# Kernel optimization log

Hardware: AMD Instinct MI355X
Metric: run time of the kernel (lower is better)

Reference implementation:

```python
import jax, jax.numpy as jnp
import numpy as np

S, B, C = 7, 2, 20
L_COORD, POS_CONF, POS_CLS, L_NOOBJ = 5.0, 1.0, 1.0, 0.5
IMG_SIZE, GRID_SIZE = 448.0, 64.0
EPS = 1e-6


def setup_inputs() -> dict:
    key = jax.random.key(0)
    k1, k2 = jax.random.split(key)
    N = 16384
    predictions = jax.random.uniform(k1, (N, S, S, B * 5 + C), dtype=jnp.float32)
    target = jax.random.uniform(k2, (N, S, S, 5 + C), dtype=jnp.float32)
    return {"predictions": predictions, "target": target}


def _iou(pred_boxes, gt_boxes, gx, gy):
    # pred_boxes: [N,S,S,B,4] (x,y offsets in cell, w,h rel. to image)
    # gt_boxes:   [N,S,S,1,4]
    # gx, gy:     broadcastable grid indices [1,S,S,1]
    def corners(b):
        cx = (gx + b[..., 0]) * GRID_SIZE   # absolute center x (pixels)
        cy = (gy + b[..., 1]) * GRID_SIZE
        w = b[..., 2] * IMG_SIZE
        h = b[..., 3] * IMG_SIZE
        return cx - w / 2, cy - h / 2, cx + w / 2, cy + h / 2, w * h

    px1, py1, px2, py2, pa = corners(pred_boxes)
    gx1, gy1, gx2, gy2, ga = corners(gt_boxes)
    iw = jnp.clip(jnp.minimum(px2, gx2) - jnp.maximum(px1, gx1), 0.0)
    ih = jnp.clip(jnp.minimum(py2, gy2) - jnp.maximum(py1, gy1), 0.0)
    inter = iw * ih
    union = pa + ga - inter
    return inter / (union + EPS)   # [N,S,S,B]


def reference(predictions, target):
    N = predictions.shape[0]
    pred_boxes = predictions[..., : B * 5].reshape(N, S, S, B, 5)
    pred_cls = predictions[..., B * 5:]          # [N,S,S,C]
    gt_box = target[..., :5][..., None, :]       # [N,S,S,1,5]
    gt_cls = target[..., 5:]                     # [N,S,S,C]

    obj = (target[..., 4] > 0.5).astype(predictions.dtype)  # [N,S,S]

    gx = jnp.arange(S, dtype=predictions.dtype)[None, None, :, None]  # col index
    gy = jnp.arange(S, dtype=predictions.dtype)[None, :, None, None]  # row index

    iou = _iou(pred_boxes[..., :4], gt_box[..., :4], gx, gy)  # [N,S,S,B]

    # responsible box: max-IoU predictor per obj cell
    resp = jax.nn.one_hot(jnp.argmax(iou, axis=-1), B, dtype=predictions.dtype)  # [N,S,S,B]
    resp_obj = resp * obj[..., None]

    # coordinate loss (x, y, sqrt(w), sqrt(h))
    dxy = jnp.sum((pred_boxes[..., :2] - gt_box[..., :2]) ** 2, axis=-1)
    dwh = jnp.sum((jnp.sqrt(jnp.clip(pred_boxes[..., 2:4], 0.0))
                   - jnp.sqrt(jnp.clip(gt_box[..., 2:4], 0.0))) ** 2, axis=-1)
    loss_coord = L_COORD * jnp.sum(resp_obj * (dxy + dwh))

    # confidence loss: responsible box targets its IoU; others target 0
    conf = pred_boxes[..., 4]
    iou_t = jax.lax.stop_gradient(iou)
    loss_conf_obj = POS_CONF * jnp.sum(resp_obj * (conf - iou_t) ** 2)
    loss_conf_noobj = L_NOOBJ * jnp.sum((1.0 - resp_obj) * conf ** 2)

    # class loss on obj cells
    loss_cls = POS_CLS * jnp.sum(obj * jnp.sum((pred_cls - gt_cls) ** 2, axis=-1))

    return (loss_coord + loss_conf_obj + loss_conf_noobj + loss_cls) / N
```

## Files before the change

kernel.cpp:

```cpp
#include <hip/hip_runtime.h>


#define S7 7
#define CELL_P 30
#define CELL_T 25
#define TPB 256
#define CPB 128

__device__ __forceinline__ void gload16(const void* g, void* l)
{
    __builtin_amdgcn_global_load_lds(
        (const __attribute__((address_space(1))) unsigned int*)g,
        (__attribute__((address_space(3))) unsigned int*)l, 16, 0, 0);
}

__global__ __launch_bounds__(TPB) void yolo_cell_kernel(
    const float* __restrict__ pred, const float* __restrict__ tgt,
    float* __restrict__ partial)
{
    __shared__ float sp[CPB * CELL_P];
    __shared__ float st[CPB * CELL_T];
    __shared__ float sred[4];

    const int t    = threadIdx.x;
    const int lane = t & 63;
    const int wid  = t >> 6;
    const int bid  = blockIdx.x;

    const char* P = (const char*)(pred + (size_t)bid * CPB * CELL_P);
    const char* T = (const char*)(tgt  + (size_t)bid * CPB * CELL_T);

    if (wid == 0 && lane < 32)
        gload16(T + 12288 + lane * 16, (char*)st + 12288);
    #pragma unroll
    for (int i = 0; i < 4; ++i) {
        int c = wid + 4 * i;
        if (c < 15) gload16(P + c * 1024 + lane * 16, (char*)sp + c * 1024);
    }
    #pragma unroll
    for (int i = 0; i < 3; ++i) {
        int c = wid + 4 * i;
        gload16(T + c * 1024 + lane * 16, (char*)st + c * 1024);
    }
    __syncthreads();

    float acc = 0.0f;
    const int cib = (wid & 1) * 64 + lane;
    const float* pv = sp + cib * CELL_P;
    const float* tv = st + cib * CELL_T;

    if (wid < 2) {
        int cell = bid * CPB + cib;
        int rem  = cell % 49;
        float gx = (float)(rem % S7);
        float gy = (float)(rem / S7);

        float obj = (tv[4] > 0.5f) ? 1.0f : 0.0f;

        float gcx = (gx + tv[0]) * 64.0f;
        float gcy = (gy + tv[1]) * 64.0f;
        float gw  = tv[2] * 448.0f;
        float gh  = tv[3] * 448.0f;
        float gx1 = gcx - gw * 0.5f, gy1 = gcy - gh * 0.5f;
        float gx2 = gcx + gw * 0.5f, gy2 = gcy + gh * 0.5f;
        float ga  = gw * gh;

        float iou[2], dxy[2], dwh[2], conf[2];
        #pragma unroll
        for (int b = 0; b < 2; ++b) {
            float b0 = pv[b * 5 + 0], b1 = pv[b * 5 + 1], b2 = pv[b * 5 + 2];
            float b3 = pv[b * 5 + 3], b4 = pv[b * 5 + 4];
            float pcx = (gx + b0) * 64.0f;
            float pcy = (gy + b1) * 64.0f;
            float pw  = b2 * 448.0f;
            float ph  = b3 * 448.0f;
            float px1 = pcx - pw * 0.5f, py1 = pcy - ph * 0.5f;
            float px2 = pcx + pw * 0.5f, py2 = pcy + ph * 0.5f;
            float pa  = pw * ph;

            float iw = fmaxf(fminf(px2, gx2) - fmaxf(px1, gx1), 0.0f);
            float ih = fmaxf(fminf(py2, gy2) - fmaxf(py1, gy1), 0.0f);
            float inter = iw * ih;
            iou[b] = inter / (pa + ga - inter + 1e-6f);

            float dx = b0 - tv[0], dy = b1 - tv[1];
            dxy[b] = dx * dx + dy * dy;
            float sw = sqrtf(fmaxf(b2, 0.0f)) - sqrtf(fmaxf(tv[2], 0.0f));
            float sh = sqrtf(fmaxf(b3, 0.0f)) - sqrtf(fmaxf(tv[3], 0.0f));
            dwh[b] = sw * sw + sh * sh;
            conf[b] = b4;
        }

        int best = (iou[1] > iou[0]) ? 1 : 0;

        #pragma unroll
        for (int b = 0; b < 2; ++b) {
            float resp_obj = (b == best) ? obj : 0.0f;
            acc += 5.0f * resp_obj * (dxy[b] + dwh[b]);
            float d = conf[b] - iou[b];
            acc += resp_obj * d * d;
            acc += 0.5f * (1.0f - resp_obj) * conf[b] * conf[b];
        }
    } else {
        float obj = (tv[4] > 0.5f) ? 1.0f : 0.0f;
        float cls = 0.0f;
        #pragma unroll
        for (int c = 0; c < 20; ++c) {
            float d = pv[10 + c] - tv[5 + c];
            cls += d * d;
        }
        acc = obj * cls;
    }

    #pragma unroll
    for (int off = 32; off > 0; off >>= 1)
        acc += __shfl_down(acc, off, 64);
    if (lane == 0) sred[wid] = acc;
    __syncthreads();
    if (t == 0) partial[bid] = sred[0] + sred[1] + sred[2] + sred[3];
}

__global__ __launch_bounds__(1024) void yolo_final_kernel(
    const float* __restrict__ partial, int n4, float* __restrict__ out, float invN)
{
    const float4* p4 = reinterpret_cast<const float4*>(partial);
    float s = 0.0f;
    for (int i = threadIdx.x; i < n4; i += 1024) {
        float4 v = p4[i];
        s += (v.x + v.y) + (v.z + v.w);
    }
    #pragma unroll
    for (int off = 32; off > 0; off >>= 1)
        s += __shfl_down(s, off, 64);

    __shared__ float smem[16];
    int lane = threadIdx.x & 63;
    int wid  = threadIdx.x >> 6;
    if (lane == 0) smem[wid] = s;
    __syncthreads();
    if (threadIdx.x == 0) {
        float r = 0.0f;
        #pragma unroll
        for (int w = 0; w < 16; ++w) r += smem[w];
        out[0] = r * invN;
    }
}

extern "C" void kernel_launch(void* const* d_in, const int* in_sizes, int n_in,
                              void* d_out, int out_size, void* d_ws, size_t ws_size,
                              hipStream_t stream)
{
    const float* pred = (const float*)d_in[0];
    const float* tgt  = (const float*)d_in[1];
    float* out        = (float*)d_out;
    float* partial    = (float*)d_ws;

    int ncells  = in_sizes[0] / CELL_P;
    int N       = ncells / 49;
    int nblocks = ncells / CPB;

    yolo_cell_kernel<<<nblocks, TPB, 0, stream>>>(pred, tgt, partial);
    yolo_final_kernel<<<1, 1024, 0, stream>>>(partial, nblocks / 4, out,
                                              1.0f / (float)N);
}
```

Before: 33.36 us.

## Make each wave load and process its own cell slice, dropping block barrier

Each wavefront now copies a contiguous 32-cell slice of predictions and targets into LDS and waits only on its own vector-memory counter instead of a block-wide __syncthreads. Within the wave, lanes 0-31 compute box/confidence terms and lanes 32-63 compute class terms for the same 32 cells. This removes the inter-wave barrier before compute. It also creates intra-wave divergence between the two halves and relies on the LDS-direct loads being complete after vmcnt(0) without an LDS barrier.

New measurement: 33.52 us. About the same (+0.5%).

```diff
diff --git a/kernel.cpp b/kernel.cpp
--- a/kernel.cpp
+++ b/kernel.cpp
@@ -6,6 +6,8 @@
 #define CELL_T 25
 #define TPB 256
 #define CPB 128
+#define PW_B 3840
+#define TW_B 3200
 
 __device__ __forceinline__ void gload16(const void* g, void* l)
 {
@@ -27,35 +29,37 @@
     const int wid  = t >> 6;
     const int bid  = blockIdx.x;
 
-    const char* P = (const char*)(pred + (size_t)bid * CPB * CELL_P);
-    const char* T = (const char*)(tgt  + (size_t)bid * CPB * CELL_T);
+    const char* P = (const char*)(pred + (size_t)bid * CPB * CELL_P) + wid * PW_B;
+    const char* T = (const char*)(tgt  + (size_t)bid * CPB * CELL_T) + wid * TW_B;
+    char* LP = (char*)sp + wid * PW_B;
+    char* LT = (char*)st + wid * TW_B;
 
-    if (wid == 0 && lane < 32)
-        gload16(T + 12288 + lane * 16, (char*)st + 12288);
     #pragma unroll
-    for (int i = 0; i < 4; ++i) {
-        int c = wid + 4 * i;
-        if (c < 15) gload16(P + c * 1024 + lane * 16, (char*)sp + c * 1024);
-    }
+    for (int k = 0; k < 3; ++k)
+        gload16(P + k * 1024 + lane * 16, LP + k * 1024);
+    if (lane < 48)
+        gload16(P + 3072 + lane * 16, LP + 3072);
     #pragma unroll
-    for (int i = 0; i < 3; ++i) {
-        int c = wid + 4 * i;
-        gload16(T + c * 1024 + lane * 16, (char*)st + c * 1024);
-    }
-    __syncthreads();
+    for (int k = 0; k < 3; ++k)
+        gload16(T + k * 1024 + lane * 16, LT + k * 1024);
+    if (lane < 8)
+        gload16(T + 3072 + lane * 16, LT + 3072);
+
+    asm volatile("s_waitcnt vmcnt(0)" ::: "memory");
+    __builtin_amdgcn_sched_barrier(0);
+
+    const int cl = lane & 31;
+    const float* pv = sp + (wid * 32 + cl) * CELL_P;
+    const float* tv = st + (wid * 32 + cl) * CELL_T;
 
     float acc = 0.0f;
-    const int cib = (wid & 1) * 64 + lane;
-    const float* pv = sp + cib * CELL_P;
-    const float* tv = st + cib * CELL_T;
+    float obj = (tv[4] > 0.5f) ? 1.0f : 0.0f;
 
-    if (wid < 2) {
-        int cell = bid * CPB + cib;
+    if (lane < 32) {
+        int cell = bid * CPB + wid * 32 + cl;
         int rem  = cell % 49;
         float gx = (float)(rem % S7);
         float gy = (float)(rem / S7);
-
-        float obj = (tv[4] > 0.5f) ? 1.0f : 0.0f;
 
         float gcx = (gx + tv[0]) * 64.0f;
         float gcy = (gy + tv[1]) * 64.0f;
@@ -102,7 +106,6 @@
             acc += 0.5f * (1.0f - resp_obj) * conf[b] * conf[b];
         }
     } else {
-        float obj = (tv[4] > 0.5f) ? 1.0f : 0.0f;
         float cls = 0.0f;
         #pragma unroll
         for (int c = 0; c < 20; ++c) {
```
